# Performance work log

Hardware: AMD Instinct MI355X
Metric: run time of the kernel (lower is better)

## Reference

```python
import jax, jax.numpy as jnp
import numpy as np

B, F, V, D, K = 16384, 39, 30000, 16, 20
EPS = 1e-5


def bn_eval(x, g, b):
    # inference-mode BatchNorm1d with running_mean=0, running_var=1
    return g * x / jnp.sqrt(1.0 + EPS) + b


def setup_inputs() -> dict:
    key = jax.random.key(0)
    ks = jax.random.split(key, 12)
    x = jax.random.randint(ks[0], (B, F), 0, V)
    emb_table = jax.random.normal(ks[1], (F * V, D), dtype=jnp.float32) * 0.05
    w_c = jax.random.normal(ks[2], (F, F * D), dtype=jnp.float32) * 0.05
    w0 = jax.random.normal(ks[3], (1024, F * D), dtype=jnp.float32) * 0.04
    w1 = jax.random.normal(ks[4], (512, 1024), dtype=jnp.float32) * 0.03
    w_out = jax.random.normal(ks[5], (1, 512), dtype=jnp.float32) * 0.04
    return {
        'x': x, 'emb_table': emb_table,
        'w_c': w_c, 'b_c': jnp.zeros((F,)), 'g_c': jnp.ones((F,)), 'be_c': jnp.zeros((F,)),
        'w0': w0, 'b0': jnp.zeros((1024,)), 'g0': jnp.ones((1024,)), 'be0': jnp.zeros((1024,)),
        'w1': w1, 'b1': jnp.zeros((512,)), 'g1': jnp.ones((512,)), 'be1': jnp.zeros((512,)),
        'w_out': w_out, 'b_out': jnp.zeros((1,)),
    }


def reference(x, emb_table, w_c, b_c, g_c, be_c, w0, b0, g0, be0,
              w1, b1, g1, be1, w_out, b_out):
    offsets = jnp.arange(F, dtype=x.dtype) * V          # per-field offsets
    idx = x + offsets[None, :]                          # [B, F]
    emb = emb_table[idx]                                # [B, F, D] gather

    # controller_mlp: flatten (batch, D, F) layout like torch transpose(1,2)
    flat = jnp.transpose(emb, (0, 2, 1)).reshape(B, F * D)
    h = jax.nn.relu(bn_eval(flat @ w_c.T + b_c, g_c, be_c))
    scores = jax.nn.softmax(h, axis=1)                  # [B, F]

    # kmax_pooling: top-k field indices, sorted ascending, gather weights
    _, kidx = jax.lax.top_k(scores, K)
    kidx = jnp.sort(kidx, axis=1)                       # [B, K]
    w = jnp.take_along_axis(scores, kidx, axis=1)       # [B, K]

    # forward_select: gather selected field embeddings, weight them
    sel = jnp.take_along_axis(emb, kidx[:, :, None], axis=1)  # [B, K, D]
    weighted = sel * w[:, :, None]

    # scatter back into full field slots (unselected fields are zero)
    full = jnp.zeros((B, F, D), weighted.dtype)
    bidx = jnp.arange(B)[:, None]
    full = full.at[bidx, kidx].set(weighted)            # [B, F, D]

    z = jnp.transpose(full, (0, 2, 1)).reshape(B, F * D)
    z = jax.nn.relu(bn_eval(z @ w0.T + b0, g0, be0))
    z = jax.nn.relu(bn_eval(z @ w1.T + b1, g1, be1))
    out = jax.nn.sigmoid(z @ w_out.T + b_out)           # [B, 1]
    return out.squeeze(-1)
```

## Files before the change

### kernel.cpp

```cpp
#include <hip/hip_runtime.h>
#include <math.h>

#define B_SZ 16384
#define F_N 39
#define V_N 30000
#define D_N 16
#define K_SEL 20
#define FD 624
#define KP0 640
#define NCP 48
#define N0 1024
#define N1 512
#define CBR 64
#define ALD 648

typedef unsigned short u16;
typedef __attribute__((ext_vector_type(8))) short bf16x8;
typedef __attribute__((ext_vector_type(8))) unsigned short u16x8;
typedef __attribute__((ext_vector_type(4))) float f32x4;

__device__ __forceinline__ u16 f2bf(float v) {
    union { float f; unsigned u; } x; x.f = v;
    unsigned r = x.u + 0x7fff + ((x.u >> 16) & 1);
    return (u16)(r >> 16);
}
__device__ __forceinline__ float bf2f(u16 v) {
    union { unsigned u; float f; } x; x.u = ((unsigned)v) << 16;
    return x.f;
}
__device__ __forceinline__ unsigned cvtpk2(float a, float b) {
    unsigned d;
    asm("v_cvt_pk_bf16_f32 %0, %1, %2" : "=v"(d) : "v"(a), "v"(b));
    return d;
}

#define GLD16(gp, lp) __builtin_amdgcn_global_load_lds( \
    (const __attribute__((address_space(1))) unsigned int*)(gp), \
    (__attribute__((address_space(3))) unsigned int*)(lp), 16, 0, 0)

__global__ __launch_bounds__(256) void prep_all_kernel(
    const float* __restrict__ w0, const float* __restrict__ w1,
    const float* __restrict__ w_c, const float* __restrict__ b_c,
    const float* __restrict__ g_c, const float* __restrict__ be_c,
    u16* __restrict__ w0b, u16* __restrict__ w1b, u16* __restrict__ wcb,
    float* __restrict__ bcp, float* __restrict__ gcp, float* __restrict__ becp,
    float* __restrict__ outp)
{
    __shared__ float Lb[8][624];
    const int bid = blockIdx.x;
    const int t   = threadIdx.x;

    if (bid < 134) {
        const bool is_w0 = (bid < 128);
        const int r0 = is_w0 ? bid * 8 : (bid - 128) * 8;
        const int nrows_src = is_w0 ? N0 : F_N;
        const float* __restrict__ src = is_w0 ? w0 : w_c;
        u16* __restrict__ dst = is_w0 ? w0b : wcb;

        for (int j = t; j < 8 * 156; j += 256) {
            const int row = j / 156;
            const int c4  = j - row * 156;
            const int n   = r0 + row;
            if (n < nrows_src)
                *(float4*)&Lb[row][c4 * 4] =
                    *(const float4*)&src[(size_t)n * FD + c4 * 4];
        }
        __syncthreads();

        for (int j = t; j < 8 * 320; j += 256) {
            const int row = j / 320;
            const int pr  = j - row * 320;
            const int n   = r0 + row;
            const int k0  = pr * 2;
            float v0 = 0.f, v1 = 0.f;
            if (n < nrows_src) {
                const int d0 = k0 & 15,       f0 = k0 >> 4;
                const int d1 = (k0 + 1) & 15, f1 = (k0 + 1) >> 4;
                if (f0 < F_N) v0 = Lb[row][d0 * F_N + f0];
                if (f1 < F_N) v1 = Lb[row][d1 * F_N + f1];
            }
            *(unsigned*)&dst[(size_t)n * KP0 + k0] = cvtpk2(v0, v1);
        }
        return;
    }
    if (bid < 390) {
        const size_t e0 = (size_t)(bid - 134) * 2048 + t * 8;
        float4 v0 = *(const float4*)(w1 + e0);
        float4 v1 = *(const float4*)(w1 + e0 + 4);
        uint4 o = { cvtpk2(v0.x, v0.y), cvtpk2(v0.z, v0.w),
                    cvtpk2(v1.x, v1.y), cvtpk2(v1.z, v1.w) };
        *(uint4*)(w1b + e0) = o;
        return;
    }
    if (bid < 398) {
        const size_t e0 = (size_t)(bid - 390) * 2048 + t * 8;
        float4 z = {0.f, 0.f, 0.f, 0.f};
        *(float4*)(outp + e0)     = z;
        *(float4*)(outp + e0 + 4) = z;
        return;
    }
    if (t < 3 * NCP) {
        const int which = t / NCP, n = t - which * NCP;
        float v = 0.f;
        if (n < F_N) v = (which == 0) ? b_c[n] : (which == 1) ? g_c[n] : be_c[n];
        ((which == 0) ? bcp : (which == 1) ? gcp : becp)[n] = v;
    }
}

__global__ __launch_bounds__(256) void fused_controller_kernel(
    const int* __restrict__ x, const float* __restrict__ emb_table,
    const u16* __restrict__ wcb, const float* __restrict__ bcp,
    const float* __restrict__ gcp, const float* __restrict__ becp,
    u16* __restrict__ zb)
{
    __shared__ __align__(16) u16 Al[CBR * ALD];
    __shared__ float vv[CBR][49];
    __shared__ float selw[CBR][F_N];

    const int t    = threadIdx.x;
    const int wave = t >> 6;
    const int lane = t & 63;
    const int b0   = blockIdx.x * CBR;

    {
        int xi[10];
        #pragma unroll
        for (int s = 0; s < 10; ++s) {
            const int p = t + s * 256;
            xi[s] = (p < CBR * F_N) ? x[b0 * F_N + p] : 0;
        }
        #pragma unroll
        for (int s = 0; s < 10; ++s) {
            const int p = t + s * 256;
            if (p < CBR * F_N) {
                const int row = p / F_N;
                const int f   = p - row * F_N;
                const float4* src =
                    (const float4*)(emb_table + (size_t)(xi[s] + f * V_N) * D_N);
                float4 v0 = src[0], v1 = src[1], v2 = src[2], v3 = src[3];
                uint4 o0 = { cvtpk2(v0.x, v0.y), cvtpk2(v0.z, v0.w),
                             cvtpk2(v1.x, v1.y), cvtpk2(v1.z, v1.w) };
                uint4 o1 = { cvtpk2(v2.x, v2.y), cvtpk2(v2.z, v2.w),
                             cvtpk2(v3.x, v3.y), cvtpk2(v3.z, v3.w) };
                *(uint4*)&Al[row * ALD + f * D_N]     = o0;
                *(uint4*)&Al[row * ALD + f * D_N + 8] = o1;
            }
        }
    }
    __syncthreads();

    const int m = lane & 15;
    const int q = lane >> 4;
    const int rbase = wave * 16;
    f32x4 acc0 = {}, acc1 = {}, acc2 = {};
    {
        const u16* ap  = &Al[(rbase + m) * ALD + q * 8];
        const u16* bp0 = wcb + (size_t)(0  + m) * KP0 + q * 8;
        const u16* bp1 = wcb + (size_t)(16 + m) * KP0 + q * 8;
        const u16* bp2 = wcb + (size_t)(32 + m) * KP0 + q * 8;
        #pragma unroll
        for (int k = 0; k < 20; ++k) {
            bf16x8 af = *(const bf16x8*)ap;
            bf16x8 b0 = *(const bf16x8*)bp0;
            bf16x8 b1 = *(const bf16x8*)bp1;
            bf16x8 b2 = *(const bf16x8*)bp2;
            acc0 = __builtin_amdgcn_mfma_f32_16x16x32_bf16(af, b0, acc0, 0, 0, 0);
            acc1 = __builtin_amdgcn_mfma_f32_16x16x32_bf16(af, b1, acc1, 0, 0, 0);
            acc2 = __builtin_amdgcn_mfma_f32_16x16x32_bf16(af, b2, acc2, 0, 0, 0);
            ap += 32; bp0 += 32; bp1 += 32; bp2 += 32;
        }
    }

    {
        const float rs = rsqrtf(1.0f + 1e-5f);
        #pragma unroll
        for (int j = 0; j < 3; ++j) {
            const f32x4 a = (j == 0) ? acc0 : (j == 1) ? acc1 : acc2;
            const int n = j * 16 + m;
            const float gn = gcp[n] * rs;
            const float bn = becp[n];
            const float bi = bcp[n];
            #pragma unroll
            for (int r = 0; r < 4; ++r)
                vv[rbase + q * 4 + r][n] = fmaxf(fmaf(gn, a[r] + bi, bn), 0.f);
        }
    }

    for (int pass = 0; pass < 4; ++pass) {
        const int row = rbase + pass * 4 + (lane >> 4);
        const int fl  = lane & 15;
        float e[3] = {0.f, 0.f, 0.f};
        float mloc = -1e30f;
        #pragma unroll
        for (int it = 0; it < 3; ++it) {
            const int f = fl + 16 * it;
            if (f < F_N) { e[it] = vv[row][f]; mloc = fmaxf(mloc, e[it]); }
        }
        mloc = fmaxf(mloc, __shfl_xor(mloc, 1, 64));
        mloc = fmaxf(mloc, __shfl_xor(mloc, 2, 64));
        mloc = fmaxf(mloc, __shfl_xor(mloc, 4, 64));
        mloc = fmaxf(mloc, __shfl_xor(mloc, 8, 64));
        float sloc = 0.f;
        #pragma unroll
        for (int it = 0; it < 3; ++it) {
            const int f = fl + 16 * it;
            if (f < F_N) { e[it] = expf(e[it] - mloc); sloc += e[it]; }
        }
        sloc += __shfl_xor(sloc, 1, 64);
        sloc += __shfl_xor(sloc, 2, 64);
        sloc += __shfl_xor(sloc, 4, 64);
        sloc += __shfl_xor(sloc, 8, 64);
        const float inv = 1.f / sloc;
        #pragma unroll
        for (int it = 0; it < 3; ++it) {
            const int f = fl + 16 * it;
            if (f < F_N) vv[row][f] = e[it];
        }

        int rank[3] = {};
        for (int gg = 0; gg < F_N; ++gg) {
            const float o = vv[row][gg];
            #pragma unroll
            for (int it = 0; it < 3; ++it) {
                const int f = fl + 16 * it;
                if (f < F_N)
                    rank[it] += (o > e[it] || (o == e[it] && gg < f)) ? 1 : 0;
            }
        }
        #pragma unroll
        for (int it = 0; it < 3; ++it) {
            const int f = fl + 16 * it;
            if (f < F_N)
                selw[row][f] = (rank[it] < K_SEL) ? e[it] * inv : 0.f;
        }
    }

    for (int gp = lane; gp < 16 * 40; gp += 64) {
        const int row  = gp / 40;
        const int slot = gp - row * 40;
        const int gr   = rbase + row;
        u16* dst = zb + (size_t)(b0 + gr) * KP0 + slot * D_N;
        uint4 o0 = {0u,0u,0u,0u}, o1 = {0u,0u,0u,0u};
        if (slot < F_N) {
            const float w = selw[gr][slot];
            u16x8 a0 = *(u16x8*)&Al[gr * ALD + slot * D_N];
            u16x8 a1 = *(u16x8*)&Al[gr * ALD + slot * D_N + 8];
            o0 = (uint4){ cvtpk2(bf2f(a0[0]) * w, bf2f(a0[1]) * w),
                          cvtpk2(bf2f(a0[2]) * w, bf2f(a0[3]) * w),
                          cvtpk2(bf2f(a0[4]) * w, bf2f(a0[5]) * w),
                          cvtpk2(bf2f(a0[6]) * w, bf2f(a0[7]) * w) };
            o1 = (uint4){ cvtpk2(bf2f(a1[0]) * w, bf2f(a1[1]) * w),
                          cvtpk2(bf2f(a1[2]) * w, bf2f(a1[3]) * w),
                          cvtpk2(bf2f(a1[4]) * w, bf2f(a1[5]) * w),
                          cvtpk2(bf2f(a1[6]) * w, bf2f(a1[7]) * w) };
        }
        *(uint4*)dst       = o0;
        *(uint4*)(dst + 8) = o1;
    }
}

template<int MODE>
__global__ __launch_bounds__(512) void gemm_mfma_bn_relu(
    const u16* __restrict__ A, const u16* __restrict__ W,
    const float* __restrict__ bias, const float* __restrict__ g,
    const float* __restrict__ be, u16* __restrict__ Cout,
    int M, int N, int Kp,
    const float* __restrict__ w_out, float* __restrict__ outp)
{
    __shared__ __align__(16) u16 SM[3 * 12288];

    const int t    = threadIdx.x;
    const int wave = t >> 6;
    const int lane = t & 63;
    const int wm   = wave >> 2, wn = wave & 3;
    const int m0   = blockIdx.x * 128;
    const int n0   = blockIdx.y * 256;

    const int rA  = t >> 2;
    const int cA  = (t & 3) ^ ((rA >> 1) & 3);
    const int rB1 = 128 + rA;
    const int cB1 = (t & 3) ^ ((rB1 >> 1) & 3);
    const u16* gA  = A + (size_t)(m0 + rA)  * Kp + cA  * 8;
    const u16* gB0 = W + (size_t)(n0 + rA)  * Kp + cA  * 8;
    const u16* gB1 = W + (size_t)(n0 + rB1) * Kp + cB1 * 8;
    const int dA = t * 8, dB0 = 4096 + t * 8, dB1 = 8192 + t * 8;

    const int q    = lane >> 4;
    const int lr16 = lane & 15;

    int aoff[4], boff[4];
    #pragma unroll
    for (int i = 0; i < 4; ++i) {
        int ra = wm * 64 + i * 16 + lr16;
        aoff[i] = ra * 32 + ((q ^ ((ra >> 1) & 3)) * 8);
        int rb = wn * 64 + i * 16 + lr16;
        boff[i] = 4096 + rb * 32 + ((q ^ ((rb >> 1) & 3)) * 8);
    }

    const int NIT = Kp >> 5;

    GLD16(gA,  SM + dA);
    GLD16(gB0, SM + dB0);
    GLD16(gB1, SM + dB1);
    gA += 32; gB0 += 32; gB1 += 32;
    GLD16(gA,  SM + 12288 + dA);
    GLD16(gB0, SM + 12288 + dB0);
    GLD16(gB1, SM + 12288 + dB1);
    gA += 32; gB0 += 32; gB1 += 32;

    f32x4 acc[4][4] = {};
    int cur = 0, stg = 2;

    for (int it = 0; it < NIT - 1; ++it) {
        asm volatile("s_waitcnt vmcnt(3)" ::: "memory");
        __builtin_amdgcn_s_barrier();
        __builtin_amdgcn_sched_barrier(0);

        const u16* ac = SM + cur * 12288;

        bf16x8 af0 = *(const bf16x8*)(ac + aoff[0]);
        bf16x8 af1 = *(const bf16x8*)(ac + aoff[1]);
        bf16x8 b0v = *(const bf16x8*)(ac + boff[0]);
        bf16x8 b1v = *(const bf16x8*)(ac + boff[1]);
        bf16x8 b2v = *(const bf16x8*)(ac + boff[2]);
        bf16x8 b3v = *(const bf16x8*)(ac + boff[3]);

        if (it + 2 < NIT) {
            u16* s = SM + stg * 12288;
            GLD16(gA,  s + dA);
            GLD16(gB0, s + dB0);
            GLD16(gB1, s + dB1);
            gA += 32; gB0 += 32; gB1 += 32;
        }

        asm volatile("s_waitcnt lgkmcnt(0)" ::: "memory");
        __builtin_amdgcn_sched_barrier(0);
        __builtin_amdgcn_s_setprio(1);
        acc[0][0] = __builtin_amdgcn_mfma_f32_16x16x32_bf16(af0, b0v, acc[0][0], 0, 0, 0);
        acc[0][1] = __builtin_amdgcn_mfma_f32_16x16x32_bf16(af0, b1v, acc[0][1], 0, 0, 0);
        acc[0][2] = __builtin_amdgcn_mfma_f32_16x16x32_bf16(af0, b2v, acc[0][2], 0, 0, 0);
        acc[0][3] = __builtin_amdgcn_mfma_f32_16x16x32_bf16(af0, b3v, acc[0][3], 0, 0, 0);
        acc[1][0] = __builtin_amdgcn_mfma_f32_16x16x32_bf16(af1, b0v, acc[1][0], 0, 0, 0);
        acc[1][1] = __builtin_amdgcn_mfma_f32_16x16x32_bf16(af1, b1v, acc[1][1], 0, 0, 0);
        acc[1][2] = __builtin_amdgcn_mfma_f32_16x16x32_bf16(af1, b2v, acc[1][2], 0, 0, 0);
        acc[1][3] = __builtin_amdgcn_mfma_f32_16x16x32_bf16(af1, b3v, acc[1][3], 0, 0, 0);
        __builtin_amdgcn_s_setprio(0);
        __builtin_amdgcn_s_barrier();

        bf16x8 af2 = *(const bf16x8*)(ac + aoff[2]);
        bf16x8 af3 = *(const bf16x8*)(ac + aoff[3]);
        asm volatile("s_waitcnt lgkmcnt(0)" ::: "memory");
        __builtin_amdgcn_sched_barrier(0);
        __builtin_amdgcn_s_setprio(1);
        acc[2][0] = __builtin_amdgcn_mfma_f32_16x16x32_bf16(af2, b0v, acc[2][0], 0, 0, 0);
        acc[2][1] = __builtin_amdgcn_mfma_f32_16x16x32_bf16(af2, b1v, acc[2][1], 0, 0, 0);
        acc[2][2] = __builtin_amdgcn_mfma_f32_16x16x32_bf16(af2, b2v, acc[2][2], 0, 0, 0);
        acc[2][3] = __builtin_amdgcn_mfma_f32_16x16x32_bf16(af2, b3v, acc[2][3], 0, 0, 0);
        acc[3][0] = __builtin_amdgcn_mfma_f32_16x16x32_bf16(af3, b0v, acc[3][0], 0, 0, 0);
        acc[3][1] = __builtin_amdgcn_mfma_f32_16x16x32_bf16(af3, b1v, acc[3][1], 0, 0, 0);
        acc[3][2] = __builtin_amdgcn_mfma_f32_16x16x32_bf16(af3, b2v, acc[3][2], 0, 0, 0);
        acc[3][3] = __builtin_amdgcn_mfma_f32_16x16x32_bf16(af3, b3v, acc[3][3], 0, 0, 0);
        __builtin_amdgcn_s_setprio(0);

        cur = (cur == 2) ? 0 : cur + 1;
        stg = (stg == 2) ? 0 : stg + 1;
    }

    asm volatile("s_waitcnt vmcnt(0)" ::: "memory");
    __builtin_amdgcn_s_barrier();
    __builtin_amdgcn_sched_barrier(0);
    {
        const u16* ac = SM + cur * 12288;
        bf16x8 af[4], bfr[4];
        #pragma unroll
        for (int i = 0; i < 4; ++i) af[i]  = *(const bf16x8*)(ac + aoff[i]);
        #pragma unroll
        for (int j = 0; j < 4; ++j) bfr[j] = *(const bf16x8*)(ac + boff[j]);
        __builtin_amdgcn_s_setprio(1);
        #pragma unroll
        for (int i = 0; i < 4; ++i)
            #pragma unroll
            for (int j = 0; j < 4; ++j)
                acc[i][j] = __builtin_amdgcn_mfma_f32_16x16x32_bf16(
                    af[i], bfr[j], acc[i][j], 0, 0, 0);
        __builtin_amdgcn_s_setprio(0);
    }

    const float rs = rsqrtf(1.0f + 1e-5f);
    if (MODE == 0) {
        __syncthreads();
        u16* Cs = SM;
        #pragma unroll
        for (int j = 0; j < 4; ++j) {
            const int nl = wn * 64 + j * 16 + lr16;
            const int n  = n0 + nl;
            const float bn_g = g[n] * rs;
            const float bn_b = be[n];
            const float bi   = bias[n];
            #pragma unroll
            for (int i = 0; i < 4; ++i) {
                const int mlb = wm * 64 + i * 16 + q * 4;
                float v0 = fmaxf(fmaf(bn_g, acc[i][j][0] + bi, bn_b), 0.f);
                float v1 = fmaxf(fmaf(bn_g, acc[i][j][1] + bi, bn_b), 0.f);
                float v2 = fmaxf(fmaf(bn_g, acc[i][j][2] + bi, bn_b), 0.f);
                float v3 = fmaxf(fmaf(bn_g, acc[i][j][3] + bi, bn_b), 0.f);
                unsigned pA = cvtpk2(v0, v1);
                unsigned pB = cvtpk2(v2, v3);
                Cs[(mlb + 0) * 264 + nl] = (u16)pA;
                Cs[(mlb + 1) * 264 + nl] = (u16)(pA >> 16);
                Cs[(mlb + 2) * 264 + nl] = (u16)pB;
                Cs[(mlb + 3) * 264 + nl] = (u16)(pB >> 16);
            }
        }
        __syncthreads();
        #pragma unroll
        for (int s = 0; s < 8; ++s) {
            const int chunk = s * 512 + t;
            const int row   = chunk >> 5;
            const int col   = (chunk & 31) << 3;
            *(u16x8*)&Cout[(size_t)(m0 + row) * N + n0 + col] =
                *(const u16x8*)&Cs[row * 264 + col];
        }
    } else {
        float s[4][4] = {};
        #pragma unroll
        for (int j = 0; j < 4; ++j) {
            const int n = n0 + wn * 64 + j * 16 + lr16;
            const float bn_g = g[n] * rs;
            const float bn_b = be[n];
            const float bi   = bias[n];
            const float wo   = w_out[n];
            #pragma unroll
            for (int i = 0; i < 4; ++i)
                #pragma unroll
                for (int r = 0; r < 4; ++r) {
                    float v = acc[i][j][r] + bi;
                    v = fmaxf(fmaf(bn_g, v, bn_b), 0.f);
                    s[i][r] = fmaf(v, wo, s[i][r]);
                }
        }
        #pragma unroll
        for (int i = 0; i < 4; ++i)
            #pragma unroll
            for (int r = 0; r < 4; ++r) {
                float v = s[i][r];
                v += __shfl_xor(v, 1, 64);
                v += __shfl_xor(v, 2, 64);
                v += __shfl_xor(v, 4, 64);
                v += __shfl_xor(v, 8, 64);
                s[i][r] = v;
            }
        if (lr16 == 0) {
            #pragma unroll
            for (int i = 0; i < 4; ++i) {
                const int mbase = m0 + wm * 64 + i * 16 + q * 4;
                #pragma unroll
                for (int r = 0; r < 4; ++r)
                    atomicAdd(&outp[mbase + r], s[i][r]);
            }
        }
    }
}

__global__ __launch_bounds__(256) void sigmoid_kernel(
    const float* __restrict__ outp, const float* __restrict__ b_out,
    float* __restrict__ out)
{
    const int b = blockIdx.x * 256 + threadIdx.x;
    out[b] = 1.f / (1.f + expf(-(outp[b] + b_out[0])));
}

extern "C" void kernel_launch(void* const* d_in, const int* in_sizes, int n_in,
                              void* d_out, int out_size, void* d_ws, size_t ws_size,
                              hipStream_t stream)
{
    const int*   x     = (const int*)  d_in[0];
    const float* emb   = (const float*)d_in[1];
    const float* w_c   = (const float*)d_in[2];
    const float* b_c   = (const float*)d_in[3];
    const float* g_c   = (const float*)d_in[4];
    const float* be_c  = (const float*)d_in[5];
    const float* w0    = (const float*)d_in[6];
    const float* b0    = (const float*)d_in[7];
    const float* g0    = (const float*)d_in[8];
    const float* be0   = (const float*)d_in[9];
    const float* w1    = (const float*)d_in[10];
    const float* b1    = (const float*)d_in[11];
    const float* g1    = (const float*)d_in[12];
    const float* be1   = (const float*)d_in[13];
    const float* w_out = (const float*)d_in[14];
    const float* b_out = (const float*)d_in[15];
    float* out = (float*)d_out;

    u16*   zb    = (u16*)d_ws;
    u16*   w0b   = zb    + (size_t)B_SZ * KP0;
    u16*   h0b   = w0b   + (size_t)N0 * KP0;
    u16*   w1b   = h0b   + (size_t)B_SZ * N0;
    u16*   wcb   = w1b   + (size_t)N1 * N0;
    float* outp  = (float*)(wcb + (size_t)NCP * KP0);
    float* bcp   = outp + B_SZ;
    float* gcp   = bcp + NCP;
    float* becp  = gcp + NCP;

    prep_all_kernel<<<399, 256, 0, stream>>>(
        w0, w1, w_c, b_c, g_c, be_c, w0b, w1b, wcb, bcp, gcp, becp, outp);

    fused_controller_kernel<<<B_SZ / CBR, 256, 0, stream>>>(
        x, emb, wcb, bcp, gcp, becp, zb);

    gemm_mfma_bn_relu<0><<<dim3(B_SZ / 128, N0 / 256), 512, 0, stream>>>(
        zb, w0b, b0, g0, be0, h0b, B_SZ, N0, KP0, nullptr, nullptr);

    gemm_mfma_bn_relu<1><<<dim3(B_SZ / 128, N1 / 256), 512, 0, stream>>>(
        h0b, w1b, b1, g1, be1, nullptr, B_SZ, N1, N0, w_out, outp);

    sigmoid_kernel<<<B_SZ / 256, 256, 0, stream>>>(outp, b_out, out);
}
```

Before: 223.1 us.

## Split embedding gather into own kernel and use split-K controller with smaller blocks

Moves the random embedding gather into a separate fully parallel kernel that writes bf16 rows to a workspace buffer. The controller kernel now handles 16 rows per block, so there are four times as many blocks. Each wave computes a K-slice of the controller GEMM, and the partial sums are reduced through shared memory. The goal is more parallelism and better latency hiding for the gather and controller stages, at the cost of an extra global round-trip and an extra kernel launch.

```diff
diff --git a/kernel.cpp b/kernel.cpp
--- a/kernel.cpp
+++ b/kernel.cpp
@@ -11,7 +11,7 @@
 #define NCP 48
 #define N0 1024
 #define N1 512
-#define CBR 64
+#define CBR 16
 #define ALD 648
 
 typedef unsigned short u16;
@@ -107,14 +107,33 @@
     }
 }
 
+__global__ __launch_bounds__(256) void gather_kernel(
+    const int* __restrict__ x, const float* __restrict__ emb_table,
+    u16* __restrict__ gb)
+{
+    const int p = blockIdx.x * 256 + threadIdx.x;
+    const int b = p / F_N;
+    const int f = p - b * F_N;
+    const int xi = x[p];
+    const float4* src = (const float4*)(emb_table + (size_t)(xi + f * V_N) * D_N);
+    float4 v0 = src[0], v1 = src[1], v2 = src[2], v3 = src[3];
+    uint4 o0 = { cvtpk2(v0.x, v0.y), cvtpk2(v0.z, v0.w),
+                 cvtpk2(v1.x, v1.y), cvtpk2(v1.z, v1.w) };
+    uint4 o1 = { cvtpk2(v2.x, v2.y), cvtpk2(v2.z, v2.w),
+                 cvtpk2(v3.x, v3.y), cvtpk2(v3.z, v3.w) };
+    u16* dst = gb + (size_t)b * KP0 + f * D_N;
+    *(uint4*)dst       = o0;
+    *(uint4*)(dst + 8) = o1;
+}
+
 __global__ __launch_bounds__(256) void fused_controller_kernel(
-    const int* __restrict__ x, const float* __restrict__ emb_table,
-    const u16* __restrict__ wcb, const float* __restrict__ bcp,
-    const float* __restrict__ gcp, const float* __restrict__ becp,
-    u16* __restrict__ zb)
+    const u16* __restrict__ gb, const u16* __restrict__ wcb,
+    const float* __restrict__ bcp, const float* __restrict__ gcp,
+    const float* __restrict__ becp, u16* __restrict__ zb)
 {
     __shared__ __align__(16) u16 Al[CBR * ALD];
     __shared__ float vv[CBR][49];
+    __shared__ f32x4 part[4][64][3];
     __shared__ float selw[CBR][F_N];
 
     const int t    = threadIdx.x;
@@ -122,44 +141,28 @@
     const int lane = t & 63;
     const int b0   = blockIdx.x * CBR;
 
-    {
-        int xi[10];
-        #pragma unroll
-        for (int s = 0; s < 10; ++s) {
-            const int p = t + s * 256;
-            xi[s] = (p < CBR * F_N) ? x[b0 * F_N + p] : 0;
-        }
-        #pragma unroll
-        for (int s = 0; s < 10; ++s) {
-            const int p = t + s * 256;
-            if (p < CBR * F_N) {
-                const int row = p / F_N;
-                const int f   = p - row * F_N;
-                const float4* src =
-                    (const float4*)(emb_table + (size_t)(xi[s] + f * V_N) * D_N);
-                float4 v0 = src[0], v1 = src[1], v2 = src[2], v3 = src[3];
-                uint4 o0 = { cvtpk2(v0.x, v0.y), cvtpk2(v0.z, v0.w),
-                             cvtpk2(v1.x, v1.y), cvtpk2(v1.z, v1.w) };
-                uint4 o1 = { cvtpk2(v2.x, v2.y), cvtpk2(v2.z, v2.w),
-                             cvtpk2(v3.x, v3.y), cvtpk2(v3.z, v3.w) };
-                *(uint4*)&Al[row * ALD + f * D_N]     = o0;
-                *(uint4*)&Al[row * ALD + f * D_N + 8] = o1;
-            }
-        }
+    #pragma unroll
+    for (int s = 0; s < 5; ++s) {
+        const int j   = t + s * 256;
+        const int row = j / 80;
+        const int c   = j - row * 80;
+        uint4 v = {0u, 0u, 0u, 0u};
+        if (c < 78)
+            v = *(const uint4*)&gb[(size_t)(b0 + row) * KP0 + c * 8];
+        *(uint4*)&Al[row * ALD + c * 8] = v;
     }
     __syncthreads();
 
     const int m = lane & 15;
     const int q = lane >> 4;
-    const int rbase = wave * 16;
     f32x4 acc0 = {}, acc1 = {}, acc2 = {};
     {
-        const u16* ap  = &Al[(rbase + m) * ALD + q * 8];
-        const u16* bp0 = wcb + (size_t)(0  + m) * KP0 + q * 8;
-        const u16* bp1 = wcb + (size_t)(16 + m) * KP0 + q * 8;
-        const u16* bp2 = wcb + (size_t)(32 + m) * KP0 + q * 8;
-        #pragma unroll
-        for (int k = 0; k < 20; ++k) {
+        const u16* ap  = &Al[m * ALD + wave * 160 + q * 8];
+        const u16* bp0 = wcb + (size_t)(0  + m) * KP0 + wave * 160 + q * 8;
+        const u16* bp1 = wcb + (size_t)(16 + m) * KP0 + wave * 160 + q * 8;
+        const u16* bp2 = wcb + (size_t)(32 + m) * KP0 + wave * 160 + q * 8;
+        #pragma unroll
+        for (int k = 0; k < 5; ++k) {
             bf16x8 af = *(const bf16x8*)ap;
             bf16x8 b0 = *(const bf16x8*)bp0;
             bf16x8 b1 = *(const bf16x8*)bp1;
@@ -170,24 +173,35 @@
             ap += 32; bp0 += 32; bp1 += 32; bp2 += 32;
         }
     }
+    part[wave][lane][0] = acc0;
+    part[wave][lane][1] = acc1;
+    part[wave][lane][2] = acc2;
+    __syncthreads();
 
     {
+        f32x4 r0 = part[0][lane][0] + part[1][lane][0] + part[2][lane][0] + part[3][lane][0];
+        f32x4 r1 = part[0][lane][1] + part[1][lane][1] + part[2][lane][1] + part[3][lane][1];
+        f32x4 r2 = part[0][lane][2] + part[1][lane][2] + part[2][lane][2] + part[3][lane][2];
+
         const float rs = rsqrtf(1.0f + 1e-5f);
-        #pragma unroll
-        for (int j = 0; j < 3; ++j) {
-            const f32x4 a = (j == 0) ? acc0 : (j == 1) ? acc1 : acc2;
-            const int n = j * 16 + m;
-            const float gn = gcp[n] * rs;
-            const float bn = becp[n];
-            const float bi = bcp[n];
-            #pragma unroll
-            for (int r = 0; r < 4; ++r)
-                vv[rbase + q * 4 + r][n] = fmaxf(fmaf(gn, a[r] + bi, bn), 0.f);
-        }
-    }
-
-    for (int pass = 0; pass < 4; ++pass) {
-        const int row = rbase + pass * 4 + (lane >> 4);
+        if (q == wave) {
+            #pragma unroll
+            for (int j = 0; j < 3; ++j) {
+                const f32x4 a = (j == 0) ? r0 : (j == 1) ? r1 : r2;
+                const int n = j * 16 + m;
+                const float gn = gcp[n] * rs;
+                const float bn = becp[n];
+                const float bi = bcp[n];
+                #pragma unroll
+                for (int r = 0; r < 4; ++r)
+                    vv[wave * 4 + r][n] = fmaxf(fmaf(gn, a[r] + bi, bn), 0.f);
+            }
+        }
+    }
+    __syncthreads();
+
+    {
+        const int row = wave * 4 + (lane >> 4);
         const int fl  = lane & 15;
         float e[3] = {0.f, 0.f, 0.f};
         float mloc = -1e30f;
@@ -234,17 +248,17 @@
                 selw[row][f] = (rank[it] < K_SEL) ? e[it] * inv : 0.f;
         }
     }
-
-    for (int gp = lane; gp < 16 * 40; gp += 64) {
+    __syncthreads();
+
+    for (int gp = t; gp < CBR * 40; gp += 256) {
         const int row  = gp / 40;
         const int slot = gp - row * 40;
-        const int gr   = rbase + row;
-        u16* dst = zb + (size_t)(b0 + gr) * KP0 + slot * D_N;
+        u16* dst = zb + (size_t)(b0 + row) * KP0 + slot * D_N;
         uint4 o0 = {0u,0u,0u,0u}, o1 = {0u,0u,0u,0u};
         if (slot < F_N) {
-            const float w = selw[gr][slot];
-            u16x8 a0 = *(u16x8*)&Al[gr * ALD + slot * D_N];
-            u16x8 a1 = *(u16x8*)&Al[gr * ALD + slot * D_N + 8];
+            const float w = selw[row][slot];
+            u16x8 a0 = *(u16x8*)&Al[row * ALD + slot * D_N];
+            u16x8 a1 = *(u16x8*)&Al[row * ALD + slot * D_N + 8];
             o0 = (uint4){ cvtpk2(bf2f(a0[0]) * w, bf2f(a0[1]) * w),
                           cvtpk2(bf2f(a0[2]) * w, bf2f(a0[3]) * w),
                           cvtpk2(bf2f(a0[4]) * w, bf2f(a0[5]) * w),
@@ -501,12 +515,15 @@
     float* bcp   = outp + B_SZ;
     float* gcp   = bcp + NCP;
     float* becp  = gcp + NCP;
+    u16*   gb    = (u16*)(becp + NCP);
 
     prep_all_kernel<<<399, 256, 0, stream>>>(
         w0, w1, w_c, b_c, g_c, be_c, w0b, w1b, wcb, bcp, gcp, becp, outp);
 
+    gather_kernel<<<(B_SZ * F_N) / 256, 256, 0, stream>>>(x, emb, gb);
+
     fused_controller_kernel<<<B_SZ / CBR, 256, 0, stream>>>(
-        x, emb, wcb, bcp, gcp, becp, zb);
+        gb, wcb, bcp, gcp, becp, zb);
 
     gemm_mfma_bn_relu<0><<<dim3(B_SZ / 128, N0 / 256), 512, 0, stream>>>(
         zb, w0b, b0, g0, be0, h0b, B_SZ, N0, KP0, nullptr, nullptr);
```

After: 219.2 us. No clear change (-1.8%).
